# Kernel optimization log

Measured on AMD Instinct MI355X. Metric: run time of the kernel, lower is better.

## Reference

```python
import jax, jax.numpy as jnp
import numpy as np

B, D_IN, D_OUT, E, TOP_K = 8192, 1024, 512, 8, 2  # D_OUT here is gate hidden = D_IN//2
OUT_DIM = 1024
LN_EPS = 1e-5


def setup_inputs() -> dict:
    key = jax.random.key(0)
    ks = jax.random.split(key, 5)
    s_in = 1.0 / np.sqrt(D_IN)
    s_h = 1.0 / np.sqrt(D_OUT)
    return {
        "x": jax.random.normal(ks[0], (B, D_IN), jnp.float32),
        "gate_w1": jax.random.normal(ks[1], (D_IN, D_OUT), jnp.float32) * s_in,
        "gate_b1": jnp.zeros((D_OUT,), jnp.float32),
        "gate_w2": jax.random.normal(ks[2], (D_OUT, E), jnp.float32) * s_h,
        "gate_b2": jnp.zeros((E,), jnp.float32),
        "We": jax.random.normal(ks[3], (E, D_IN, OUT_DIM), jnp.float32) * s_in,
        "be": jnp.zeros((E, OUT_DIM), jnp.float32),
        "ln_g": jnp.ones((E, OUT_DIM), jnp.float32),
        "ln_b": jnp.zeros((E, OUT_DIM), jnp.float32),
    }


def reference(x, gate_w1, gate_b1, gate_w2, gate_b2, We, be, ln_g, ln_b):
    # Gating network: Linear -> GELU (exact) -> Linear
    g = jax.nn.gelu(x @ gate_w1 + gate_b1, approximate=False)
    scores = g @ gate_w2 + gate_b2                       # [B, E]
    topk_s, topk_i = jax.lax.top_k(scores, TOP_K)        # [B, K]
    topk_w = jax.nn.softmax(topk_s, axis=-1)             # softmax over the top-k only
    # Scatter top-k weights into dense per-expert weights [B, E]
    rows = jnp.arange(scores.shape[0])[:, None]
    dense_w = jnp.zeros_like(scores).at[rows, topk_i].add(topk_w)
    # All-expert forward (non-selected experts get weight 0): Linear -> LayerNorm -> GELU
    h = jnp.einsum("bi,eio->beo", x, We) + be            # [B, E, O]
    mu = h.mean(axis=-1, keepdims=True)
    var = jnp.mean(jnp.square(h - mu), axis=-1, keepdims=True)
    h = (h - mu) * jax.lax.rsqrt(var + LN_EPS) * ln_g + ln_b
    h = jax.nn.gelu(h, approximate=False)
    # Weighted combine (Dropout is identity in eval mode)
    return jnp.einsum("beo,be->bo", h, dense_w)          # [B, O]
```

## Files before the change

kernel.cpp:

```cpp
#include <hip/hip_runtime.h>
#include <hip/hip_bf16.h>
#include <math.h>

#define B_ROWS 8192
#define D_INK  1024
#define D_H    512
#define N_E    8
#define OUT_D  1024
#define LN_EPS 1e-5f
#define GAP_TAU 3e-3f

typedef _Float16 f16x8 __attribute__((ext_vector_type(8)));
typedef _Float16 f16x4v __attribute__((ext_vector_type(4)));
typedef float    f32x4  __attribute__((ext_vector_type(4)));

#define GLOBAL_AS __attribute__((address_space(1)))
#define LDS_AS    __attribute__((address_space(3)))

__device__ __forceinline__ void async16(const void* gptr, void* lptr) {
  __builtin_amdgcn_global_load_lds((const GLOBAL_AS unsigned int*)gptr,
                                   (LDS_AS unsigned int*)lptr, 16, 0, 0);
}

__device__ __forceinline__ float gelu_exact(float x) {
  return 0.5f * x * (1.0f + erff(x * 0.707106781186547524f));
}
__device__ __forceinline__ float clamp_diag(float v) {
  return fminf(fmaxf(v, -1e15f), 1e15f);
}

__global__ __launch_bounds__(256) void convert_x_kernel(
    const float4* __restrict__ x4, f16x4v* __restrict__ hi4) {
  int i = blockIdx.x * 256 + threadIdx.x;
  float4 v = x4[i];
  f16x4v h;
  h[0] = (_Float16)v.x; h[1] = (_Float16)v.y;
  h[2] = (_Float16)v.z; h[3] = (_Float16)v.w;
  hi4[i] = h;
}

__global__ void transpose_split_kernel(const float* __restrict__ src,
                                       _Float16* __restrict__ hi,
                                       int R, int C) {
  __shared__ float tile[32][33];
  long base = (long)blockIdx.z * R * C;
  int c0 = blockIdx.x * 32, r0 = blockIdx.y * 32;
  int tx = threadIdx.x, ty = threadIdx.y;
#pragma unroll
  for (int i = ty; i < 32; i += 8)
    tile[i][tx] = src[base + (long)(r0 + i) * C + (c0 + tx)];
  __syncthreads();
#pragma unroll
  for (int i = ty; i < 32; i += 8)
    hi[base + (long)(c0 + i) * R + (r0 + tx)] = (_Float16)tile[tx][i];
}


__global__ __launch_bounds__(256) void gate_gemm_kernel(
    const _Float16* __restrict__ xh, const _Float16* __restrict__ wh,
    const float* __restrict__ b1, float* __restrict__ g) {
  __shared__ __align__(16) unsigned short Ah[128 * 64];
  __shared__ __align__(16) unsigned short Bh[128 * 64];
  int tid = threadIdx.x, lane = tid & 63, wave = tid >> 6;
  int wm = wave >> 1, wn = wave & 1;
  int n0 = blockIdx.x * 128, m0 = blockIdx.y * 128;

  const char* pah[4]; const char* pbh[4];
#pragma unroll
  for (int i = 0; i < 4; ++i) {
    int f = i * 256 + tid;
    int rowt = f >> 3, slot = f & 7;
    int seg = slot ^ (rowt & 7);
    pah[i] = (const char*)xh + (long)(m0 + rowt) * (D_INK * 2) + seg * 16;
    pbh[i] = (const char*)wh + (long)(n0 + rowt) * (D_INK * 2) + seg * 16;
  }
  f32x4 acc[4][4];
#pragma unroll
  for (int mi = 0; mi < 4; ++mi)
#pragma unroll
    for (int ni = 0; ni < 4; ++ni) acc[mi][ni] = (f32x4){0.f, 0.f, 0.f, 0.f};

  int cl = lane & 15, quad = lane >> 4;
  for (int k0 = 0; k0 < D_INK; k0 += 64) {
#pragma unroll
    for (int i = 0; i < 4; ++i) {
      async16(pah[i] + (long)k0 * 2, (char*)Ah + (i * 256 + wave * 64) * 16);
      async16(pbh[i] + (long)k0 * 2, (char*)Bh + (i * 256 + wave * 64) * 16);
    }
    __syncthreads();
#pragma unroll
    for (int ks = 0; ks < 2; ++ks) {
      f16x8 ah[4], bh[4];
#pragma unroll
      for (int mi = 0; mi < 4; ++mi) {
        int row = wm * 64 + mi * 16 + cl;
        ah[mi] = *(const f16x8*)((const char*)Ah + row * 128 +
                                 (((ks * 4 + quad) ^ (cl & 7)) * 16));
      }
#pragma unroll
      for (int ni = 0; ni < 4; ++ni) {
        int row = wn * 64 + ni * 16 + cl;
        bh[ni] = *(const f16x8*)((const char*)Bh + row * 128 +
                                 (((ks * 4 + quad) ^ (cl & 7)) * 16));
      }
#pragma unroll
      for (int mi = 0; mi < 4; ++mi)
#pragma unroll
        for (int ni = 0; ni < 4; ++ni)
          acc[mi][ni] = __builtin_amdgcn_mfma_f32_16x16x32_f16(ah[mi], bh[ni], acc[mi][ni], 0, 0, 0);
    }
    __syncthreads();
  }
#pragma unroll
  for (int mi = 0; mi < 4; ++mi)
#pragma unroll
    for (int r = 0; r < 4; ++r) {
      int row = m0 + wm * 64 + mi * 16 + quad * 4 + r;
#pragma unroll
      for (int ni = 0; ni < 4; ++ni) {
        int col = n0 + wn * 64 + ni * 16 + cl;
        float v = clamp_diag(acc[mi][ni][r] + b1[col]);
        g[(long)row * D_H + col] = gelu_exact(v);
      }
    }
}

__global__ __launch_bounds__(256) void score_kernel(
    const float* __restrict__ g, const float* __restrict__ w2,
    const float* __restrict__ b2, float* __restrict__ scores,
    int* __restrict__ nflag, int* __restrict__ worklist) {
  int tid = threadIdx.x, lane = tid & 63, wave = tid >> 6;
  int b = blockIdx.x * 4 + wave;
  const float* grow = g + (long)b * D_H + lane * 8;
  float4 g0 = *(const float4*)grow;
  float4 g1 = *(const float4*)(grow + 4);
  float gv[8] = {g0.x, g0.y, g0.z, g0.w, g1.x, g1.y, g1.z, g1.w};
  float acc[8];
#pragma unroll
  for (int e = 0; e < 8; ++e) acc[e] = 0.f;
#pragma unroll
  for (int j = 0; j < 8; ++j) {
    const float* wrow = w2 + (lane * 8 + j) * N_E;
#pragma unroll
    for (int e = 0; e < 8; ++e) acc[e] += gv[j] * wrow[e];
  }
#pragma unroll
  for (int off = 32; off >= 1; off >>= 1)
#pragma unroll
    for (int e = 0; e < 8; ++e) acc[e] += __shfl_xor(acc[e], off, 64);
  if (lane == 0) {
    float s[8];
#pragma unroll
    for (int e = 0; e < 8; ++e) { s[e] = acc[e] + b2[e]; scores[b * N_E + e] = s[e]; }
    int i0 = 0;
#pragma unroll
    for (int e = 1; e < 8; ++e) if (s[e] > s[i0]) i0 = e;
    int i1 = (i0 == 0) ? 1 : 0;
#pragma unroll
    for (int e = 0; e < 8; ++e) if (e != i0 && s[e] > s[i1]) i1 = e;
    float s2 = -3e38f;
#pragma unroll
    for (int e = 0; e < 8; ++e) if (e != i0 && e != i1 && s[e] > s2) s2 = s[e];
    if (s[i1] - s2 < GAP_TAU) {
      int idx = atomicAdd(nflag, 1);
      worklist[idx] = b;
    }
  }
}

__global__ __launch_bounds__(256) void fixup_g_kernel(
    const float* __restrict__ x, const float* __restrict__ w1,
    const float* __restrict__ b1, const int* __restrict__ nflag,
    const int* __restrict__ worklist, double* __restrict__ g64) {
  int n = *nflag;
  int total = n * 2;
  for (int t = blockIdx.x; t < total; t += gridDim.x) {
    int w = t >> 1, half = t & 1;
    int row = worklist[w];
    int col = half * 256 + threadIdx.x;
    const float* xr = x + (long)row * D_INK;
    double a0 = 0.0, a1 = 0.0, a2 = 0.0, a3 = 0.0;
    for (int k = 0; k < D_INK; k += 4) {
      a0 += (double)xr[k + 0] * (double)w1[(long)(k + 0) * D_H + col];
      a1 += (double)xr[k + 1] * (double)w1[(long)(k + 1) * D_H + col];
      a2 += (double)xr[k + 2] * (double)w1[(long)(k + 2) * D_H + col];
      a3 += (double)xr[k + 3] * (double)w1[(long)(k + 3) * D_H + col];
    }
    double s = ((a0 + a1) + (a2 + a3)) + (double)b1[col];
    g64[(long)w * D_H + col] = 0.5 * s * (1.0 + erf(s * 0.70710678118654752440));
  }
}

__global__ __launch_bounds__(256) void fixup_score_kernel(
    const double* __restrict__ g64, const float* __restrict__ w2,
    const float* __restrict__ b2, const int* __restrict__ nflag,
    const int* __restrict__ worklist, float* __restrict__ scores) {
  __shared__ double p2[256];
  int n = *nflag;
  int tid = threadIdx.x;
  for (int w = blockIdx.x; w < n; w += gridDim.x) {
    int row = worklist[w];
    int e = tid & 7, seg = tid >> 3;
    double s = 0.0;
#pragma unroll
    for (int q = seg * 16; q < seg * 16 + 16; ++q)
      s += g64[(long)w * D_H + q] * (double)w2[q * N_E + e];
    p2[tid] = s;
    __syncthreads();
    if (tid < N_E) {
      double t = 0.0;
      for (int i = 0; i < 32; ++i) t += p2[i * 8 + tid];
      scores[row * N_E + tid] = (float)(t + (double)b2[tid]);
    }
    __syncthreads();
  }
}

__global__ __launch_bounds__(256) void select_kernel(
    const float* __restrict__ scores, int* __restrict__ counts,
    int* __restrict__ bucket, float* __restrict__ pair_w,
    int* __restrict__ pair_e) {
  __shared__ int lcnt[N_E];
  __shared__ int lbase[N_E];
  int tid = threadIdx.x;
  int b = blockIdx.x * 256 + tid;
  if (tid < N_E) lcnt[tid] = 0;
  __syncthreads();
  float s[8];
#pragma unroll
  for (int e = 0; e < 8; ++e) s[e] = scores[b * N_E + e];
  int i0 = 0;
#pragma unroll
  for (int e = 1; e < 8; ++e) if (s[e] > s[i0]) i0 = e;
  int i1 = (i0 == 0) ? 1 : 0;
#pragma unroll
  for (int e = 0; e < 8; ++e) if (e != i0 && s[e] > s[i1]) i1 = e;
  float z = expf(s[i1] - s[i0]);
  float inv = 1.0f / (1.0f + z);
  int r0 = atomicAdd(&lcnt[i0], 1);
  int r1 = atomicAdd(&lcnt[i1], 1);
  __syncthreads();
  if (tid < N_E) lbase[tid] = atomicAdd(&counts[tid], lcnt[tid]);
  __syncthreads();
  int p0 = 2 * b, p1 = 2 * b + 1;
  pair_e[p0] = i0; pair_w[p0] = inv;
  pair_e[p1] = i1; pair_w[p1] = z * inv;
  bucket[i0 * B_ROWS + lbase[i0] + r0] = p0;
  bucket[i1 * B_ROWS + lbase[i1] + r1] = p1;
}

__global__ __launch_bounds__(256) void expert_gemm_kernel(
    const _Float16* __restrict__ xh, const _Float16* __restrict__ wet,
    const int* __restrict__ counts, const int* __restrict__ bucket,
    __bf16* __restrict__ h) {
  int nt = blockIdx.x, mt = blockIdx.y, e = blockIdx.z;
  int cnt = counts[e];
  if (mt * 128 >= cnt) return;
  __shared__ __align__(16) unsigned short As[128 * 64];
  __shared__ __align__(16) unsigned short Bs[128 * 64];
  __shared__ int dest_s[128];
  int tid = threadIdx.x, lane = tid & 63, wave = tid >> 6;
  int wm = wave >> 1, wn = wave & 1;
  int n0 = nt * 128;
  if (tid < 128) {
    int idx = mt * 128 + tid;
    dest_s[tid] = (idx < cnt) ? bucket[e * B_ROWS + idx] : 0;
  }
  __syncthreads();
  const char* xb = (const char*)xh;
  const char* wb = (const char*)wet + (long)e * (D_INK * OUT_D * 2);
  const char* aptr[4];
  const char* bptr[4];
#pragma unroll
  for (int i = 0; i < 4; ++i) {
    int f = i * 256 + tid;
    int rowt = f >> 3, slot = f & 7;
    int seg = slot ^ (rowt & 7);
    int rowid = dest_s[rowt] >> 1;
    aptr[i] = xb + (long)rowid * (D_INK * 2) + seg * 16;
    bptr[i] = wb + (long)(n0 + rowt) * (D_INK * 2) + seg * 16;
  }
  f32x4 acc[4][4];
#pragma unroll
  for (int mi = 0; mi < 4; ++mi)
#pragma unroll
    for (int ni = 0; ni < 4; ++ni) acc[mi][ni] = (f32x4){0.f, 0.f, 0.f, 0.f};

  int cl = lane & 15, quad = lane >> 4;
  for (int k0 = 0; k0 < D_INK; k0 += 64) {
#pragma unroll
    for (int i = 0; i < 4; ++i) {
      async16(aptr[i] + (long)k0 * 2, (char*)As + (i * 256 + wave * 64) * 16);
      async16(bptr[i] + (long)k0 * 2, (char*)Bs + (i * 256 + wave * 64) * 16);
    }
    __syncthreads();
#pragma unroll
    for (int ks = 0; ks < 2; ++ks) {
      f16x8 af[4], bfr[4];
#pragma unroll
      for (int mi = 0; mi < 4; ++mi) {
        int row = wm * 64 + mi * 16 + cl;
        af[mi] = *(const f16x8*)((const char*)As + row * 128 +
                                 (((ks * 4 + quad) ^ (cl & 7)) * 16));
      }
#pragma unroll
      for (int ni = 0; ni < 4; ++ni) {
        int row = wn * 64 + ni * 16 + cl;
        bfr[ni] = *(const f16x8*)((const char*)Bs + row * 128 +
                                  (((ks * 4 + quad) ^ (cl & 7)) * 16));
      }
#pragma unroll
      for (int mi = 0; mi < 4; ++mi)
#pragma unroll
        for (int ni = 0; ni < 4; ++ni)
          acc[mi][ni] = __builtin_amdgcn_mfma_f32_16x16x32_f16(af[mi], bfr[ni], acc[mi][ni], 0, 0, 0);
    }
    __syncthreads();
  }
#pragma unroll
  for (int mi = 0; mi < 4; ++mi)
#pragma unroll
    for (int r = 0; r < 4; ++r) {
      int row128 = wm * 64 + mi * 16 + quad * 4 + r;
      if (mt * 128 + row128 < cnt) {
        long dest = dest_s[row128];
        __bf16* hp = h + dest * OUT_D + n0 + wn * 64 + cl;
#pragma unroll
        for (int ni = 0; ni < 4; ++ni)
          hp[ni * 16] = (__bf16)clamp_diag(acc[mi][ni][r]);
      }
    }
}

__global__ __launch_bounds__(256) void ln_combine_kernel(
    const __bf16* __restrict__ h, const float* __restrict__ pair_w,
    const int* __restrict__ pair_e, const float* __restrict__ be,
    const float* __restrict__ ln_g, const float* __restrict__ ln_b,
    float* __restrict__ out) {
  int b = blockIdx.x, tid = threadIdx.x;
  int lane = tid & 63, wave = tid >> 6;
  __shared__ float red[4][4];
  float hv[2][4];
  float stats[4];
  int ei[2]; float wi[2];
#pragma unroll
  for (int k = 0; k < 2; ++k) {
    int p = 2 * b + k;
    ei[k] = pair_e[p]; wi[k] = pair_w[p];
    const __bf16* hp = h + (long)p * OUT_D;
    const float* bep = be + ei[k] * OUT_D;
    float s = 0.f, sq = 0.f;
#pragma unroll
    for (int j = 0; j < 4; ++j) {
      int col = tid + j * 256;
      float v = (float)hp[col] + bep[col];
      hv[k][j] = v; s += v; sq += v * v;
    }
    stats[2 * k] = s; stats[2 * k + 1] = sq;
  }
#pragma unroll
  for (int off = 32; off >= 1; off >>= 1)
#pragma unroll
    for (int i = 0; i < 4; ++i) stats[i] += __shfl_xor(stats[i], off, 64);
  if (lane == 0) {
#pragma unroll
    for (int i = 0; i < 4; ++i) red[wave][i] = stats[i];
  }
  __syncthreads();
  float tot[4] = {0.f, 0.f, 0.f, 0.f};
#pragma unroll
  for (int w = 0; w < 4; ++w)
#pragma unroll
    for (int i = 0; i < 4; ++i) tot[i] += red[w][i];
  float outv[4] = {0.f, 0.f, 0.f, 0.f};
#pragma unroll
  for (int k = 0; k < 2; ++k) {
    float mean = tot[2 * k] * (1.0f / OUT_D);
    float var = tot[2 * k + 1] * (1.0f / OUT_D) - mean * mean;
    float rstd = rsqrtf(fmaxf(var, 0.f) + LN_EPS);
    const float* gp = ln_g + ei[k] * OUT_D;
    const float* bp = ln_b + ei[k] * OUT_D;
#pragma unroll
    for (int j = 0; j < 4; ++j) {
      int col = tid + j * 256;
      float t = (hv[k][j] - mean) * rstd * gp[col] + bp[col];
      outv[j] += wi[k] * gelu_exact(t);
    }
  }
#pragma unroll
  for (int j = 0; j < 4; ++j)
    out[(long)b * OUT_D + tid + j * 256] = outv[j];
}

extern "C" void kernel_launch(void* const* d_in, const int* in_sizes, int n_in,
                              void* d_out, int out_size, void* d_ws, size_t ws_size,
                              hipStream_t stream) {
  const float* x       = (const float*)d_in[0];
  const float* gate_w1 = (const float*)d_in[1];
  const float* gate_b1 = (const float*)d_in[2];
  const float* gate_w2 = (const float*)d_in[3];
  const float* gate_b2 = (const float*)d_in[4];
  const float* We      = (const float*)d_in[5];
  const float* be      = (const float*)d_in[6];
  const float* ln_g    = (const float*)d_in[7];
  const float* ln_b    = (const float*)d_in[8];
  float* out = (float*)d_out;

  char* ws = (char*)d_ws;
  size_t off = 0;
  _Float16* x16h = (_Float16*)(ws + off); off += (size_t)B_ROWS * D_INK * 2;
  _Float16* w1th = (_Float16*)(ws + off); off += (size_t)D_H * D_INK * 2;
  _Float16* wet  = (_Float16*)(ws + off); off += (size_t)N_E * D_INK * OUT_D * 2;
  float* g       = (float*)(ws + off); off += (size_t)B_ROWS * D_H * 4;
  float* scores  = (float*)(ws + off); off += (size_t)B_ROWS * N_E * 4;
  int* counts    = (int*)(ws + off);   off += 64;
  int* nflag     = counts + 8;
  int* worklist  = (int*)(ws + off);   off += (size_t)B_ROWS * 4;
  int* bucket    = (int*)(ws + off);   off += (size_t)N_E * B_ROWS * 4;
  float* pair_w  = (float*)(ws + off); off += (size_t)2 * B_ROWS * 4;
  int* pair_e    = (int*)(ws + off);   off += (size_t)2 * B_ROWS * 4;
  __bf16* h      = (__bf16*)(ws + off); off += (size_t)2 * B_ROWS * OUT_D * 2;
  double* g64    = (double*)h;

  hipMemsetAsync(counts, 0, 64, stream);
  convert_x_kernel<<<B_ROWS * D_INK / 4 / 256, 256, 0, stream>>>(
      (const float4*)x, (f16x4v*)x16h);
  transpose_split_kernel<<<dim3(D_H / 32, D_INK / 32, 1), dim3(32, 8), 0, stream>>>(
      gate_w1, w1th, D_INK, D_H);
  transpose_split_kernel<<<dim3(OUT_D / 32, D_INK / 32, N_E), dim3(32, 8), 0, stream>>>(
      We, wet, D_INK, OUT_D);
  gate_gemm_kernel<<<dim3(D_H / 128, B_ROWS / 128), 256, 0, stream>>>(
      x16h, w1th, gate_b1, g);
  score_kernel<<<B_ROWS / 4, 256, 0, stream>>>(
      g, gate_w2, gate_b2, scores, nflag, worklist);
  fixup_g_kernel<<<512, 256, 0, stream>>>(
      x, gate_w1, gate_b1, nflag, worklist, g64);
  fixup_score_kernel<<<128, 256, 0, stream>>>(
      g64, gate_w2, gate_b2, nflag, worklist, scores);
  select_kernel<<<B_ROWS / 256, 256, 0, stream>>>(
      scores, counts, bucket, pair_w, pair_e);
  expert_gemm_kernel<<<dim3(OUT_D / 128, B_ROWS / 128, N_E), 256, 0, stream>>>(
      x16h, wet, counts, bucket, h);
  ln_combine_kernel<<<B_ROWS, 256, 0, stream>>>(
      h, pair_w, pair_e, be, ln_g, ln_b, out);
}
```

Measured before the change: 319.1 us.

## Enlarge expert GEMM tile to 256x256 and vectorize LN-combine loads

The expert GEMM moves from 128x128 tiles with 4 waves to 256x256 tiles with 8 waves, each wave computing 128x64. This raises data reuse per LDS load and cuts the number of blocks. The A fragment is now loaded per mi inside the loop to limit register pressure. The LN-combine kernel switches to contiguous 4-element-per-thread vector loads and stores, with bf16 widened by a bit shift. Costs: more LDS per block, more accumulator registers, possibly lower occupancy, and more wasted work on partially filled tiles for experts whose row count is not a multiple of 256.

```diff
diff --git a/kernel.cpp b/kernel.cpp
--- a/kernel.cpp
+++ b/kernel.cpp
@@ -249,21 +249,21 @@
   bucket[i1 * B_ROWS + lbase[i1] + r1] = p1;
 }
 
-__global__ __launch_bounds__(256) void expert_gemm_kernel(
+__global__ __launch_bounds__(512) void expert_gemm_kernel(
     const _Float16* __restrict__ xh, const _Float16* __restrict__ wet,
     const int* __restrict__ counts, const int* __restrict__ bucket,
     __bf16* __restrict__ h) {
   int nt = blockIdx.x, mt = blockIdx.y, e = blockIdx.z;
   int cnt = counts[e];
-  if (mt * 128 >= cnt) return;
-  __shared__ __align__(16) unsigned short As[128 * 64];
-  __shared__ __align__(16) unsigned short Bs[128 * 64];
-  __shared__ int dest_s[128];
+  if (mt * 256 >= cnt) return;
+  __shared__ __align__(16) unsigned short As[256 * 64];
+  __shared__ __align__(16) unsigned short Bs[256 * 64];
+  __shared__ int dest_s[256];
   int tid = threadIdx.x, lane = tid & 63, wave = tid >> 6;
-  int wm = wave >> 1, wn = wave & 1;
-  int n0 = nt * 128;
-  if (tid < 128) {
-    int idx = mt * 128 + tid;
+  int wm = wave >> 2, wn = wave & 3;
+  int n0 = nt * 256;
+  if (tid < 256) {
+    int idx = mt * 256 + tid;
     dest_s[tid] = (idx < cnt) ? bucket[e * B_ROWS + idx] : 0;
   }
   __syncthreads();
@@ -273,16 +273,16 @@
   const char* bptr[4];
 #pragma unroll
   for (int i = 0; i < 4; ++i) {
-    int f = i * 256 + tid;
+    int f = i * 512 + tid;
     int rowt = f >> 3, slot = f & 7;
     int seg = slot ^ (rowt & 7);
     int rowid = dest_s[rowt] >> 1;
     aptr[i] = xb + (long)rowid * (D_INK * 2) + seg * 16;
     bptr[i] = wb + (long)(n0 + rowt) * (D_INK * 2) + seg * 16;
   }
-  f32x4 acc[4][4];
-#pragma unroll
-  for (int mi = 0; mi < 4; ++mi)
+  f32x4 acc[8][4];
+#pragma unroll
+  for (int mi = 0; mi < 8; ++mi)
 #pragma unroll
     for (int ni = 0; ni < 4; ++ni) acc[mi][ni] = (f32x4){0.f, 0.f, 0.f, 0.f};
 
@@ -290,19 +290,13 @@
   for (int k0 = 0; k0 < D_INK; k0 += 64) {
 #pragma unroll
     for (int i = 0; i < 4; ++i) {
-      async16(aptr[i] + (long)k0 * 2, (char*)As + (i * 256 + wave * 64) * 16);
-      async16(bptr[i] + (long)k0 * 2, (char*)Bs + (i * 256 + wave * 64) * 16);
+      async16(aptr[i] + (long)k0 * 2, (char*)As + (i * 512 + wave * 64) * 16);
+      async16(bptr[i] + (long)k0 * 2, (char*)Bs + (i * 512 + wave * 64) * 16);
     }
     __syncthreads();
 #pragma unroll
     for (int ks = 0; ks < 2; ++ks) {
-      f16x8 af[4], bfr[4];
-#pragma unroll
-      for (int mi = 0; mi < 4; ++mi) {
-        int row = wm * 64 + mi * 16 + cl;
-        af[mi] = *(const f16x8*)((const char*)As + row * 128 +
-                                 (((ks * 4 + quad) ^ (cl & 7)) * 16));
-      }
+      f16x8 bfr[4];
 #pragma unroll
       for (int ni = 0; ni < 4; ++ni) {
         int row = wn * 64 + ni * 16 + cl;
@@ -310,20 +304,24 @@
                                   (((ks * 4 + quad) ^ (cl & 7)) * 16));
       }
 #pragma unroll
-      for (int mi = 0; mi < 4; ++mi)
+      for (int mi = 0; mi < 8; ++mi) {
+        int row = wm * 128 + mi * 16 + cl;
+        f16x8 af = *(const f16x8*)((const char*)As + row * 128 +
+                                   (((ks * 4 + quad) ^ (cl & 7)) * 16));
 #pragma unroll
         for (int ni = 0; ni < 4; ++ni)
-          acc[mi][ni] = __builtin_amdgcn_mfma_f32_16x16x32_f16(af[mi], bfr[ni], acc[mi][ni], 0, 0, 0);
-    }
-    __syncthreads();
-  }
-#pragma unroll
-  for (int mi = 0; mi < 4; ++mi)
+          acc[mi][ni] = __builtin_amdgcn_mfma_f32_16x16x32_f16(af, bfr[ni], acc[mi][ni], 0, 0, 0);
+      }
+    }
+    __syncthreads();
+  }
+#pragma unroll
+  for (int mi = 0; mi < 8; ++mi)
 #pragma unroll
     for (int r = 0; r < 4; ++r) {
-      int row128 = wm * 64 + mi * 16 + quad * 4 + r;
-      if (mt * 128 + row128 < cnt) {
-        long dest = dest_s[row128];
+      int row256 = wm * 128 + mi * 16 + quad * 4 + r;
+      if (mt * 256 + row256 < cnt) {
+        long dest = dest_s[row256];
         __bf16* hp = h + dest * OUT_D + n0 + wn * 64 + cl;
 #pragma unroll
         for (int ni = 0; ni < 4; ++ni)
@@ -339,6 +337,7 @@
     float* __restrict__ out) {
   int b = blockIdx.x, tid = threadIdx.x;
   int lane = tid & 63, wave = tid >> 6;
+  int c0 = tid * 4;
   __shared__ float red[4][4];
   float hv[2][4];
   float stats[4];
@@ -347,16 +346,16 @@
   for (int k = 0; k < 2; ++k) {
     int p = 2 * b + k;
     ei[k] = pair_e[p]; wi[k] = pair_w[p];
-    const __bf16* hp = h + (long)p * OUT_D;
-    const float* bep = be + ei[k] * OUT_D;
-    float s = 0.f, sq = 0.f;
-#pragma unroll
-    for (int j = 0; j < 4; ++j) {
-      int col = tid + j * 256;
-      float v = (float)hp[col] + bep[col];
-      hv[k][j] = v; s += v; sq += v * v;
-    }
-    stats[2 * k] = s; stats[2 * k + 1] = sq;
+    const unsigned short* hp = (const unsigned short*)(h + (long)p * OUT_D) + c0;
+    ushort4 raw = *(const ushort4*)hp;
+    float4 bev = *(const float4*)(be + ei[k] * OUT_D + c0);
+    float v0 = __uint_as_float((unsigned)raw.x << 16) + bev.x;
+    float v1 = __uint_as_float((unsigned)raw.y << 16) + bev.y;
+    float v2 = __uint_as_float((unsigned)raw.z << 16) + bev.z;
+    float v3 = __uint_as_float((unsigned)raw.w << 16) + bev.w;
+    hv[k][0] = v0; hv[k][1] = v1; hv[k][2] = v2; hv[k][3] = v3;
+    stats[2 * k] = v0 + v1 + v2 + v3;
+    stats[2 * k + 1] = v0 * v0 + v1 * v1 + v2 * v2 + v3 * v3;
   }
 #pragma unroll
   for (int off = 32; off >= 1; off >>= 1)
@@ -378,18 +377,19 @@
     float mean = tot[2 * k] * (1.0f / OUT_D);
     float var = tot[2 * k + 1] * (1.0f / OUT_D) - mean * mean;
     float rstd = rsqrtf(fmaxf(var, 0.f) + LN_EPS);
-    const float* gp = ln_g + ei[k] * OUT_D;
-    const float* bp = ln_b + ei[k] * OUT_D;
-#pragma unroll
-    for (int j = 0; j < 4; ++j) {
-      int col = tid + j * 256;
-      float t = (hv[k][j] - mean) * rstd * gp[col] + bp[col];
-      outv[j] += wi[k] * gelu_exact(t);
-    }
-  }
-#pragma unroll
-  for (int j = 0; j < 4; ++j)
-    out[(long)b * OUT_D + tid + j * 256] = outv[j];
+    float4 gp = *(const float4*)(ln_g + ei[k] * OUT_D + c0);
+    float4 bp = *(const float4*)(ln_b + ei[k] * OUT_D + c0);
+    float t0 = (hv[k][0] - mean) * rstd * gp.x + bp.x;
+    float t1 = (hv[k][1] - mean) * rstd * gp.y + bp.y;
+    float t2 = (hv[k][2] - mean) * rstd * gp.z + bp.z;
+    float t3 = (hv[k][3] - mean) * rstd * gp.w + bp.w;
+    outv[0] += wi[k] * gelu_exact(t0);
+    outv[1] += wi[k] * gelu_exact(t1);
+    outv[2] += wi[k] * gelu_exact(t2);
+    outv[3] += wi[k] * gelu_exact(t3);
+  }
+  float4 o; o.x = outv[0]; o.y = outv[1]; o.z = outv[2]; o.w = outv[3];
+  *(float4*)(out + (long)b * OUT_D + c0) = o;
 }
 
 extern "C" void kernel_launch(void* const* d_in, const int* in_sizes, int n_in,
@@ -439,7 +439,7 @@
       g64, gate_w2, gate_b2, nflag, worklist, scores);
   select_kernel<<<B_ROWS / 256, 256, 0, stream>>>(
       scores, counts, bucket, pair_w, pair_e);
-  expert_gemm_kernel<<<dim3(OUT_D / 128, B_ROWS / 128, N_E), 256, 0, stream>>>(
+  expert_gemm_kernel<<<dim3(OUT_D / 256, B_ROWS / 256, N_E), 512, 0, stream>>>(
       x16h, wet, counts, bucket, h);
   ln_combine_kernel<<<B_ROWS, 256, 0, stream>>>(
       h, pair_w, pair_e, be, ln_g, ln_b, out);
```

New measurement: 322.8 us. Within noise of the previous version (+1.2%).
